# Performance work log

Measured on AMD Instinct MI355X. Metric: run time of the kernel, lower is better.

The kernel has to match this reference:

```python
import jax, jax.numpy as jnp
import numpy as np


def setup_inputs() -> dict:
    key = jax.random.key(0)
    k1, k2, k3, k4 = jax.random.split(key, 4)
    B, D, H, W, M = 16, 512, 96, 96, 128
    x = jax.random.normal(k1, (B, D, H, W), dtype=jnp.float32)
    evolved_feat = jax.random.normal(k2, (B, M, D), dtype=jnp.float32)
    # 1x1 conv over 2*D channels -> 1 channel: weight [2D], bias [1]
    conv_w = jax.random.normal(k3, (2 * D,), dtype=jnp.float32) * (1.0 / np.sqrt(2 * D))
    conv_b = jax.random.normal(k4, (1,), dtype=jnp.float32) * 0.01
    return {"x": x, "evolved_feat": evolved_feat, "conv_w": conv_w, "conv_b": conv_b}


def reference(x, evolved_feat, conv_w, conv_b):
    # x: [B, D, H, W], evolved_feat: [B, M, D]
    B, D, H, W = x.shape
    M = evolved_feat.shape[1]
    # conv1x1 over concat([x_pixel, evolve_node]) == split dot products, broadcast-added
    wA, wB = conv_w[:D], conv_w[D:]
    x_flat = x.reshape(B, D, H * W).transpose(0, 2, 1)       # [B, HW, D]
    s_pix = x_flat @ wA                                      # [B, HW]
    s_node = evolved_feat @ wB                               # [B, M]
    scores = s_pix[:, :, None] + s_node[:, None, :] + conv_b[0]  # [B, HW, M]
    # original softmax is over dim=0 of the [HW, M] per-batch matrix -> axis=1 here
    mapping = jax.nn.softmax(scores, axis=1)                 # [B, HW, M]
    out = jax.nn.relu(jnp.einsum('bpm,bmd->bpd', mapping, evolved_feat))  # [B, HW, D]
    out = out.reshape(B, H, W, D).transpose(0, 3, 1, 2)      # [B, D, H, W]
    return out
```

## Files before the change

kernel.cpp:

```cpp
#include <hip/hip_runtime.h>
#include <math.h>

#define Bn 16
#define Dn 512
#define Hn 96
#define Wn 96
#define Pn (Hn * Wn)
#define Mn 128

#define DZ 16
#define DCH (Dn / DZ)
#define PC 9
#define NCHUNK 36
#define DG 4

typedef float vfloat4 __attribute__((ext_vector_type(4)));

__global__ void k_spix4(const float* __restrict__ x, const float* __restrict__ conv_w,
                        float* __restrict__ partial) {
    __shared__ float wA[DCH];
    const int b  = blockIdx.x;
    const int pc = blockIdx.y;
    const int dz = blockIdx.z;
    const int t  = threadIdx.x;
    if (t < DCH) wA[t] = conv_w[dz * DCH + t];
    __syncthreads();

    const int p = pc * 1024 + t * 4;
    const float* xb = x + ((size_t)(b * Dn + dz * DCH)) * Pn + p;
    vfloat4 acc = {0.f, 0.f, 0.f, 0.f};
#pragma unroll 8
    for (int d = 0; d < DCH; ++d) {
        vfloat4 v = __builtin_nontemporal_load((const vfloat4*)(xb + (size_t)d * Pn));
        const float wv = wA[d];
        acc.x = fmaf(v.x, wv, acc.x);
        acc.y = fmaf(v.y, wv, acc.y);
        acc.z = fmaf(v.z, wv, acc.z);
        acc.w = fmaf(v.w, wv, acc.w);
    }
    *(vfloat4*)(partial + ((size_t)(b * DZ + dz)) * Pn + p) = acc;
}

__global__ void k_finish(const float* __restrict__ partial, const float* __restrict__ ef,
                         float* __restrict__ w, float* __restrict__ pexp,
                         float* __restrict__ E) {
    __shared__ float red[256];
    const int b = blockIdx.x;
    const int c = blockIdx.y;
    const int t = threadIdx.x;
    const int p = c * 256 + t;
    const size_t base = (size_t)b * DZ * Pn + p;
    float s = 0.f;
#pragma unroll
    for (int z = 0; z < DZ; ++z) s += partial[base + (size_t)z * Pn];
    const float e = __expf(s);
    w[b * Pn + p] = e;
    red[t] = e;
    __syncthreads();
    for (int o = 128; o > 0; o >>= 1) {
        if (t < o) red[t] += red[t + o];
        __syncthreads();
    }
    if (t == 0) pexp[b * NCHUNK + c] = red[0];

    if (c < 2) {
        const int d = c * 256 + t;
        const float* q = ef + (size_t)b * Mn * Dn + d;
        float sE = 0.f;
#pragma unroll 8
        for (int m = 0; m < Mn; ++m) sE += q[(size_t)m * Dn];
        E[b * Dn + d] = sE;
    }
}

__global__ void k_out(const float* __restrict__ w, const float* __restrict__ E,
                      const float* __restrict__ pexp, float* __restrict__ out) {
    const int b  = blockIdx.x;
    const int dg = blockIdx.y * DG;
    const int t  = threadIdx.x;

    float denom = 0.f;
#pragma unroll
    for (int j = 0; j < NCHUNK; ++j) denom += pexp[b * NCHUNK + j];
    const float inv = 1.f / denom;

    float ev[DG];
#pragma unroll
    for (int r = 0; r < DG; ++r) ev[r] = E[b * Dn + dg + r] * inv;

    const vfloat4* w4 = (const vfloat4*)(w + b * Pn);
    vfloat4* o4 = (vfloat4*)(out + ((size_t)(b * Dn + dg)) * Pn);
#pragma unroll
    for (int i = t; i < Pn / 4; i += 256) {
        vfloat4 v = w4[i];
#pragma unroll
        for (int r = 0; r < DG; ++r) {
            vfloat4 o;
            o.x = fmaxf(v.x * ev[r], 0.f);
            o.y = fmaxf(v.y * ev[r], 0.f);
            o.z = fmaxf(v.z * ev[r], 0.f);
            o.w = fmaxf(v.w * ev[r], 0.f);
            __builtin_nontemporal_store(o, &o4[(size_t)r * (Pn / 4) + i]);
        }
    }
}

extern "C" void kernel_launch(void* const* d_in, const int* in_sizes, int n_in,
                              void* d_out, int out_size, void* d_ws, size_t ws_size,
                              hipStream_t stream) {
    const float* x      = (const float*)d_in[0];
    const float* ef     = (const float*)d_in[1];
    const float* conv_w = (const float*)d_in[2];

    float* out = (float*)d_out;

    float* w       = (float*)d_ws;
    float* E       = w + Bn * Pn;
    float* partial = E + Bn * Dn;
    float* pexp    = partial + (size_t)Bn * DZ * Pn;
    (void)in_sizes; (void)n_in; (void)out_size; (void)ws_size;

    k_spix4<<<dim3(Bn, PC, DZ), dim3(256), 0, stream>>>(x, conv_w, partial);

    k_finish<<<dim3(Bn, NCHUNK), dim3(256), 0, stream>>>(partial, ef, w, pexp, E);

    k_out<<<dim3(Bn, Dn / DG), dim3(256), 0, stream>>>(w, E, pexp, out);
}
```

Before: 120.2 us.

## Give each s_pix block a full pixel row with register-blocked accumulators

The pixel-score reduction kernel changes from a grid of (batch, pixel-chunk, channel-slice) blocks to (batch, channel-slice) blocks. Each thread now keeps nine float4 accumulators and walks whole 9216-pixel rows for 16 channels, so nine independent loads are in flight per channel step. The channel split doubles from 16 to 32 slices. This doubles the partial-sum buffer that k_finish must read, and it cuts the grid to 512 blocks, which may leave too few waves per CU to hide memory latency.

```diff
diff --git a/kernel.cpp b/kernel.cpp
--- a/kernel.cpp
+++ b/kernel.cpp
@@ -8,37 +8,44 @@
 #define Pn (Hn * Wn)
 #define Mn 128
 
-#define DZ 16
+#define DZ 32
 #define DCH (Dn / DZ)
-#define PC 9
+#define NJ 9
 #define NCHUNK 36
 #define DG 4
 
 typedef float vfloat4 __attribute__((ext_vector_type(4)));
 
-__global__ void k_spix4(const float* __restrict__ x, const float* __restrict__ conv_w,
-                        float* __restrict__ partial) {
+__global__ void k_spix_seq(const float* __restrict__ x, const float* __restrict__ conv_w,
+                           float* __restrict__ partial) {
     __shared__ float wA[DCH];
     const int b  = blockIdx.x;
-    const int pc = blockIdx.y;
-    const int dz = blockIdx.z;
+    const int dz = blockIdx.y;
     const int t  = threadIdx.x;
     if (t < DCH) wA[t] = conv_w[dz * DCH + t];
     __syncthreads();
 
-    const int p = pc * 1024 + t * 4;
-    const float* xb = x + ((size_t)(b * Dn + dz * DCH)) * Pn + p;
-    vfloat4 acc = {0.f, 0.f, 0.f, 0.f};
-#pragma unroll 8
+    const float* xb = x + ((size_t)(b * Dn + dz * DCH)) * Pn + t * 4;
+    vfloat4 acc[NJ];
+#pragma unroll
+    for (int j = 0; j < NJ; ++j) acc[j] = (vfloat4){0.f, 0.f, 0.f, 0.f};
+
     for (int d = 0; d < DCH; ++d) {
-        vfloat4 v = __builtin_nontemporal_load((const vfloat4*)(xb + (size_t)d * Pn));
+        const float* row = xb + (size_t)d * Pn;
         const float wv = wA[d];
-        acc.x = fmaf(v.x, wv, acc.x);
-        acc.y = fmaf(v.y, wv, acc.y);
-        acc.z = fmaf(v.z, wv, acc.z);
-        acc.w = fmaf(v.w, wv, acc.w);
+#pragma unroll
+        for (int j = 0; j < NJ; ++j) {
+            vfloat4 v = __builtin_nontemporal_load((const vfloat4*)(row + j * 1024));
+            acc[j].x = fmaf(v.x, wv, acc[j].x);
+            acc[j].y = fmaf(v.y, wv, acc[j].y);
+            acc[j].z = fmaf(v.z, wv, acc[j].z);
+            acc[j].w = fmaf(v.w, wv, acc[j].w);
+        }
     }
-    *(vfloat4*)(partial + ((size_t)(b * DZ + dz)) * Pn + p) = acc;
+
+    float* pb = partial + ((size_t)(b * DZ + dz)) * Pn + t * 4;
+#pragma unroll
+    for (int j = 0; j < NJ; ++j) *(vfloat4*)(pb + j * 1024) = acc[j];
 }
 
 __global__ void k_finish(const float* __restrict__ partial, const float* __restrict__ ef,
@@ -120,7 +127,7 @@
     float* pexp    = partial + (size_t)Bn * DZ * Pn;
     (void)in_sizes; (void)n_in; (void)out_size; (void)ws_size;
 
-    k_spix4<<<dim3(Bn, PC, DZ), dim3(256), 0, stream>>>(x, conv_w, partial);
+    k_spix_seq<<<dim3(Bn, DZ), dim3(256), 0, stream>>>(x, conv_w, partial);
 
     k_finish<<<dim3(Bn, NCHUNK), dim3(256), 0, stream>>>(partial, ef, w, pexp, E);
 
```

Result: no change. 121.6 us (+1.1%).
